# Kernel optimization log

Hardware: AMD Instinct MI355X
Metric: run time of the kernel (lower is better)

## Reference

```python
import jax, jax.numpy as jnp
import numpy as np

VOCAB, EMB, HID, OUT = 50257, 128, 256, 32
B, S = 128, 2048


def setup_inputs() -> dict:
    key = jax.random.key(0)
    ks = jax.random.split(key, 12)
    return {
        "inputs": jax.random.randint(ks[0], (B, S), 0, VOCAB, dtype=jnp.int64) if jax.config.jax_enable_x64 else jax.random.randint(ks[0], (B, S), 0, VOCAB, dtype=jnp.int32),
        "weight": jax.random.normal(ks[1], (VOCAB, EMB), dtype=jnp.float32),
        "Wxf": jax.random.normal(ks[2], (4 * HID, EMB), dtype=jnp.float32) * 0.05,
        "bxf": jax.random.normal(ks[3], (4 * HID,), dtype=jnp.float32) * 0.05,
        "Whf": jax.random.normal(ks[4], (4 * HID, HID), dtype=jnp.float32) * 0.05,
        "bhf": jax.random.normal(ks[5], (4 * HID,), dtype=jnp.float32) * 0.05,
        "Wxb": jax.random.normal(ks[6], (4 * HID, EMB), dtype=jnp.float32) * 0.05,
        "bxb": jax.random.normal(ks[7], (4 * HID,), dtype=jnp.float32) * 0.05,
        "Whb": jax.random.normal(ks[8], (4 * HID, HID), dtype=jnp.float32) * 0.05,
        "bhb": jax.random.normal(ks[9], (4 * HID,), dtype=jnp.float32) * 0.05,
        "Why": jax.random.normal(ks[10], (OUT, HID), dtype=jnp.float32) * 0.05,
        "by": jax.random.normal(ks[11], (OUT,), dtype=jnp.float32) * 0.05,
    }


def _cell_zero_state(x, Wx, bx, Wh, bh):
    # One LSTM-cell step with h=0, c=0 (the original loop never updates state,
    # so every step sees zero h/c and only the final iteration's hy survives).
    # h2h(0) contributes only its bias bh.
    gates = x @ Wx.T + bx + bh                      # [B, 4H]
    i, f, g, o = jnp.split(gates, 4, axis=1)
    cy = jax.nn.sigmoid(i) * jnp.tanh(g)            # c=0 => forget term vanishes
    return jax.nn.sigmoid(o) * jnp.tanh(cy)         # [B, H]


def reference(inputs, weight, Wxf, bxf, Whf, bhf, Wxb, bxb, Whb, bhb, Why, by):
    emb = weight[inputs]                            # [B, S, EMB] gather (memory-bound)
    # Forward loop ends at t = S-1; backward (reversed) loop ends at t = 0.
    hy_f = _cell_zero_state(emb[:, -1], Wxf, bxf, Whf, bhf)
    hy_b = _cell_zero_state(emb[:, 0], Wxb, bxb, Whb, bhb)
    hy = hy_f + hy_b                                # [B, H]
    logits = hy @ Why.T + by                        # [B, OUT]
    return jax.nn.log_softmax(logits, axis=1)
```

## Files before the change

kernel.cpp:

```cpp
#include <hip/hip_runtime.h>
#include <math.h>

constexpr int B_   = 128;
constexpr int S_   = 2048;
constexpr int EMB_ = 128;
constexpr int HID_ = 256;
constexpr int OUT_ = 32;

constexpr int HT   = 8;
constexpr int BH   = 64;
constexpr int PADK = EMB_ + 4;


__global__ __launch_bounds__(512) void gates_gemm(
    const int*   __restrict__ inputs,
    const float* __restrict__ weight,
    const float* __restrict__ Wxf, const float* __restrict__ bxf, const float* __restrict__ bhf,
    const float* __restrict__ Wxb, const float* __restrict__ bxb, const float* __restrict__ bhb,
    float*       __restrict__ hy_ws)
{
    __shared__ __align__(16) float Xs[BH][PADK];
    __shared__ __align__(16) float Ws[3][HT][PADK];
    __shared__ int toks[BH];

    const int blk   = blockIdx.x;
    const int dir   = blk >> 6;
    const int ht    = (blk & 63) >> 1;
    const int bhalf = blk & 1;
    const int h0    = ht * HT;
    const int tid   = threadIdx.x;

    if (tid < BH)
        toks[tid] = inputs[(size_t)(bhalf * BH + tid) * S_ + (dir ? 0 : (S_ - 1))];
    __syncthreads();

    #pragma unroll
    for (int p = 0; p < 4; ++p) {
        const int idx = p * 512 + tid;
        const int bl  = idx >> 5;
        const int j   = idx & 31;
        const float4 v = reinterpret_cast<const float4*>(weight + (size_t)toks[bl] * EMB_)[j];
        *reinterpret_cast<float4*>(&Xs[bl][4 * j]) = v;
    }
    {
        const float* Wx = dir ? Wxb : Wxf;
        for (int idx = tid; idx < 3 * HT * 32; idx += 512) {
            const int g   = idx >> 8;
            const int rem = idx & 255;
            const int hl  = rem >> 5;
            const int j   = rem & 31;
            const int grow = (g == 0) ? 0 : ((g == 1) ? 2 : 3);
            const float4 v = reinterpret_cast<const float4*>(
                Wx + (size_t)(grow * HID_ + h0 + hl) * EMB_)[j];
            *reinterpret_cast<float4*>(&Ws[g][hl][4 * j]) = v;
        }
    }
    __syncthreads();

    const int hl = tid & (HT - 1);
    const int bg = tid >> 3;
    const int b  = bhalf * BH + bg;
    const int h  = h0 + hl;

    const float* bx = dir ? bxb : bxf;
    const float* bh = dir ? bhb : bhf;
    float gi = bx[h]            + bh[h];
    float gg = bx[2 * HID_ + h] + bh[2 * HID_ + h];
    float go = bx[3 * HID_ + h] + bh[3 * HID_ + h];

    #pragma unroll 8
    for (int k4 = 0; k4 < EMB_ / 4; ++k4) {
        const float4 x  = *reinterpret_cast<const float4*>(&Xs[bg][4 * k4]);
        const float4 wi = *reinterpret_cast<const float4*>(&Ws[0][hl][4 * k4]);
        const float4 wg = *reinterpret_cast<const float4*>(&Ws[1][hl][4 * k4]);
        const float4 wo = *reinterpret_cast<const float4*>(&Ws[2][hl][4 * k4]);
        gi = fmaf(x.x, wi.x, fmaf(x.y, wi.y, fmaf(x.z, wi.z, fmaf(x.w, wi.w, gi))));
        gg = fmaf(x.x, wg.x, fmaf(x.y, wg.y, fmaf(x.z, wg.z, fmaf(x.w, wg.w, gg))));
        go = fmaf(x.x, wo.x, fmaf(x.y, wo.y, fmaf(x.z, wo.z, fmaf(x.w, wo.w, go))));
    }

    const float si = 1.0f / (1.0f + expf(-gi));
    const float so = 1.0f / (1.0f + expf(-go));
    hy_ws[((size_t)dir * B_ + b) * HID_ + h] = so * tanhf(si * tanhf(gg));
}

__global__ __launch_bounds__(512) void epilogue(
    const float* __restrict__ hy_ws,
    const float* __restrict__ Why,
    const float* __restrict__ by,
    float*       __restrict__ out)
{
    __shared__ __align__(16) float hs[HID_];
    __shared__ float lg[OUT_];

    const int b   = blockIdx.x;
    const int tid = threadIdx.x;

    if (tid < HID_ / 4) {
        const float4 f = reinterpret_cast<const float4*>(hy_ws + (size_t)b * HID_)[tid];
        const float4 r = reinterpret_cast<const float4*>(hy_ws + ((size_t)B_ + b) * HID_)[tid];
        *reinterpret_cast<float4*>(&hs[4 * tid]) =
            make_float4(f.x + r.x, f.y + r.y, f.z + r.z, f.w + r.w);
    }
    __syncthreads();

    const int w    = tid >> 6;
    const int lane = tid & 63;
    #pragma unroll
    for (int i = 0; i < OUT_ / 8; ++i) {
        const int o = w + 8 * i;
        const float4 wv = reinterpret_cast<const float4*>(Why + (size_t)o * HID_)[lane];
        const float4 hv = *reinterpret_cast<const float4*>(&hs[4 * lane]);
        float p = fmaf(hv.x, wv.x, fmaf(hv.y, wv.y, fmaf(hv.z, wv.z, hv.w * wv.w)));
        #pragma unroll
        for (int off = 32; off; off >>= 1) p += __shfl_xor(p, off);
        if (lane == 0) lg[o] = p + by[o];
    }
    __syncthreads();

    if (tid < OUT_) {
        const float v = lg[tid];
        float m = v;
        #pragma unroll
        for (int off = 16; off; off >>= 1) m = fmaxf(m, __shfl_xor(m, off));
        float s = expf(v - m);
        #pragma unroll
        for (int off = 16; off; off >>= 1) s += __shfl_xor(s, off);
        out[(size_t)b * OUT_ + tid] = v - m - logf(s);
    }
}

extern "C" void kernel_launch(void* const* d_in, const int* in_sizes, int n_in,
                              void* d_out, int out_size, void* d_ws, size_t ws_size,
                              hipStream_t stream) {
    const int*   inputs = (const int*)  d_in[0];
    const float* weight = (const float*)d_in[1];
    const float* Wxf    = (const float*)d_in[2];
    const float* bxf    = (const float*)d_in[3];
    const float* bhf    = (const float*)d_in[5];
    const float* Wxb    = (const float*)d_in[6];
    const float* bxb    = (const float*)d_in[7];
    const float* bhb    = (const float*)d_in[9];
    const float* Why    = (const float*)d_in[10];
    const float* by     = (const float*)d_in[11];
    float* out = (float*)d_out;

    float* hy_ws = (float*)d_ws;

    gates_gemm<<<2 * (HID_ / HT) * 2, 512, 0, stream>>>(
        inputs, weight, Wxf, bxf, bhf, Wxb, bxb, bhb, hy_ws);
    epilogue<<<B_, 512, 0, stream>>>(hy_ws, Why, by, out);
}
```

Baseline: 13.77 us.

## Fuse gates GEMM and epilogue into one kernel with a grid barrier

Merges the two kernel launches into a single 128-block kernel. A software grid-wide barrier, built from an atomic arrival counter and an epoch flag, separates the gate computation from the per-batch projection and log-softmax. This removes one launch and the gap between kernels. In exchange, all 128 blocks must be co-resident for the spin barrier to work, and the barrier adds atomic traffic. The counter and epoch words in the workspace are never reset, so the code relies on epoch comparison and modulo arithmetic on the counter to stay correct across calls.

```diff
diff --git a/kernel.cpp b/kernel.cpp
--- a/kernel.cpp
+++ b/kernel.cpp
@@ -10,18 +10,27 @@
 constexpr int HT   = 8;
 constexpr int BH   = 64;
 constexpr int PADK = EMB_ + 4;
+constexpr int NBLK = 128;
 
+constexpr size_t EPOCH_OFF = 64;
+constexpr size_t HY_OFF    = 4096;
 
-__global__ __launch_bounds__(512) void gates_gemm(
+__global__ __launch_bounds__(512) void bilstm_fused(
     const int*   __restrict__ inputs,
     const float* __restrict__ weight,
     const float* __restrict__ Wxf, const float* __restrict__ bxf, const float* __restrict__ bhf,
     const float* __restrict__ Wxb, const float* __restrict__ bxb, const float* __restrict__ bhb,
-    float*       __restrict__ hy_ws)
+    const float* __restrict__ Why, const float* __restrict__ by,
+    unsigned int* __restrict__ ctr,
+    unsigned int* __restrict__ epoch,
+    float*        __restrict__ hy_ws,
+    float*        __restrict__ out)
 {
     __shared__ __align__(16) float Xs[BH][PADK];
     __shared__ __align__(16) float Ws[3][HT][PADK];
-    __shared__ int toks[BH];
+    __shared__ int   toks[BH];
+    __shared__ __align__(16) float hv[2][HID_];
+    __shared__ float lg[OUT_];
 
     const int blk   = blockIdx.x;
     const int dir   = blk >> 6;
@@ -57,61 +66,65 @@
     }
     __syncthreads();
 
-    const int hl = tid & (HT - 1);
-    const int bg = tid >> 3;
-    const int b  = bhalf * BH + bg;
-    const int h  = h0 + hl;
+    {
+        const int hl = tid & (HT - 1);
+        const int bg = tid >> 3;
+        const int h  = h0 + hl;
+        const float* bx = dir ? bxb : bxf;
+        const float* bh = dir ? bhb : bhf;
+        float gi = bx[h]            + bh[h];
+        float gg = bx[2 * HID_ + h] + bh[2 * HID_ + h];
+        float go = bx[3 * HID_ + h] + bh[3 * HID_ + h];
 
-    const float* bx = dir ? bxb : bxf;
-    const float* bh = dir ? bhb : bhf;
-    float gi = bx[h]            + bh[h];
-    float gg = bx[2 * HID_ + h] + bh[2 * HID_ + h];
-    float go = bx[3 * HID_ + h] + bh[3 * HID_ + h];
-
-    #pragma unroll 8
-    for (int k4 = 0; k4 < EMB_ / 4; ++k4) {
-        const float4 x  = *reinterpret_cast<const float4*>(&Xs[bg][4 * k4]);
-        const float4 wi = *reinterpret_cast<const float4*>(&Ws[0][hl][4 * k4]);
-        const float4 wg = *reinterpret_cast<const float4*>(&Ws[1][hl][4 * k4]);
-        const float4 wo = *reinterpret_cast<const float4*>(&Ws[2][hl][4 * k4]);
-        gi = fmaf(x.x, wi.x, fmaf(x.y, wi.y, fmaf(x.z, wi.z, fmaf(x.w, wi.w, gi))));
-        gg = fmaf(x.x, wg.x, fmaf(x.y, wg.y, fmaf(x.z, wg.z, fmaf(x.w, wg.w, gg))));
-        go = fmaf(x.x, wo.x, fmaf(x.y, wo.y, fmaf(x.z, wo.z, fmaf(x.w, wo.w, go))));
+        #pragma unroll 8
+        for (int k4 = 0; k4 < EMB_ / 4; ++k4) {
+            const float4 x  = *reinterpret_cast<const float4*>(&Xs[bg][4 * k4]);
+            const float4 wi = *reinterpret_cast<const float4*>(&Ws[0][hl][4 * k4]);
+            const float4 wg = *reinterpret_cast<const float4*>(&Ws[1][hl][4 * k4]);
+            const float4 wo = *reinterpret_cast<const float4*>(&Ws[2][hl][4 * k4]);
+            gi = fmaf(x.x, wi.x, fmaf(x.y, wi.y, fmaf(x.z, wi.z, fmaf(x.w, wi.w, gi))));
+            gg = fmaf(x.x, wg.x, fmaf(x.y, wg.y, fmaf(x.z, wg.z, fmaf(x.w, wg.w, gg))));
+            go = fmaf(x.x, wo.x, fmaf(x.y, wo.y, fmaf(x.z, wo.z, fmaf(x.w, wo.w, go))));
+        }
+        const float si = 1.0f / (1.0f + expf(-gi));
+        const float so = 1.0f / (1.0f + expf(-go));
+        hy_ws[((size_t)dir * B_ + (bhalf * BH + bg)) * HID_ + h] =
+            so * tanhf(si * tanhf(gg));
     }
 
-    const float si = 1.0f / (1.0f + expf(-gi));
-    const float so = 1.0f / (1.0f + expf(-go));
-    hy_ws[((size_t)dir * B_ + b) * HID_ + h] = so * tanhf(si * tanhf(gg));
-}
-
-__global__ __launch_bounds__(512) void epilogue(
-    const float* __restrict__ hy_ws,
-    const float* __restrict__ Why,
-    const float* __restrict__ by,
-    float*       __restrict__ out)
-{
-    __shared__ __align__(16) float hs[HID_];
-    __shared__ float lg[OUT_];
-
-    const int b   = blockIdx.x;
-    const int tid = threadIdx.x;
-
-    if (tid < HID_ / 4) {
-        const float4 f = reinterpret_cast<const float4*>(hy_ws + (size_t)b * HID_)[tid];
-        const float4 r = reinterpret_cast<const float4*>(hy_ws + ((size_t)B_ + b) * HID_)[tid];
-        *reinterpret_cast<float4*>(&hs[4 * tid]) =
-            make_float4(f.x + r.x, f.y + r.y, f.z + r.z, f.w + r.w);
+    __threadfence();
+    __syncthreads();
+    if (tid == 0) {
+        const unsigned int e0 = atomicAdd(epoch, 0u);
+        __threadfence();
+        const unsigned int old = atomicAdd(ctr, 1u);
+        if ((old & (NBLK - 1u)) == (NBLK - 1u)) {
+            __threadfence();
+            atomicAdd(epoch, 1u);
+        }
+        while (atomicAdd(epoch, 0u) == e0)
+            __builtin_amdgcn_s_sleep(2);
+        __threadfence();
     }
     __syncthreads();
 
-    const int w    = tid >> 6;
+    {
+        const int d = tid >> 8;
+        const int h = tid & 255;
+        hv[d][h] = hy_ws[((size_t)d * B_ + blk) * HID_ + h];
+    }
+    __syncthreads();
+
+    const int wave = tid >> 6;
     const int lane = tid & 63;
     #pragma unroll
-    for (int i = 0; i < OUT_ / 8; ++i) {
-        const int o = w + 8 * i;
+    for (int i = 0; i < 4; ++i) {
+        const int o = wave + 8 * i;
         const float4 wv = reinterpret_cast<const float4*>(Why + (size_t)o * HID_)[lane];
-        const float4 hv = *reinterpret_cast<const float4*>(&hs[4 * lane]);
-        float p = fmaf(hv.x, wv.x, fmaf(hv.y, wv.y, fmaf(hv.z, wv.z, hv.w * wv.w)));
+        const float4 a0 = *reinterpret_cast<const float4*>(&hv[0][4 * lane]);
+        const float4 a1 = *reinterpret_cast<const float4*>(&hv[1][4 * lane]);
+        float p = wv.x * (a0.x + a1.x) + wv.y * (a0.y + a1.y)
+                + wv.z * (a0.z + a1.z) + wv.w * (a0.w + a1.w);
         #pragma unroll
         for (int off = 32; off; off >>= 1) p += __shfl_xor(p, off);
         if (lane == 0) lg[o] = p + by[o];
@@ -126,7 +139,7 @@
         float s = expf(v - m);
         #pragma unroll
         for (int off = 16; off; off >>= 1) s += __shfl_xor(s, off);
-        out[(size_t)b * OUT_ + tid] = v - m - logf(s);
+        out[(size_t)blk * OUT_ + tid] = v - m - logf(s);
     }
 }
 
@@ -145,9 +158,12 @@
     const float* by     = (const float*)d_in[11];
     float* out = (float*)d_out;
 
-    float* hy_ws = (float*)d_ws;
+    unsigned int* ctr   = (unsigned int*)d_ws;
+    unsigned int* epoch = (unsigned int*)((char*)d_ws + EPOCH_OFF);
+    float*        hy_ws = (float*)((char*)d_ws + HY_OFF);
 
-    gates_gemm<<<2 * (HID_ / HT) * 2, 512, 0, stream>>>(
-        inputs, weight, Wxf, bxf, bhf, Wxb, bxb, bhb, hy_ws);
-    epilogue<<<B_, 512, 0, stream>>>(hy_ws, Why, by, out);
+    bilstm_fused<<<NBLK, 512, 0, stream>>>(inputs, weight,
+                                           Wxf, bxf, bhf,
+                                           Wxb, bxb, bhb,
+                                           Why, by, ctr, epoch, hy_ws, out);
 }
```

Result: slower. 41.85 us (+203.9%).
